# Kernel optimization log

Hardware: AMD Instinct MI355X
Metric: run time of the kernel (lower is better)

## Reference

```python
import jax, jax.numpy as jnp
import numpy as np

B, N, M = 4, 2048, 2048
QUERY_DIM = 512
CONTEXT_DIM = 512
HEADS = 8
DIM_HEAD = 64
INNER = HEADS * DIM_HEAD  # 512
SCALE = DIM_HEAD ** -0.5


def setup_inputs() -> dict:
    key = jax.random.key(0)
    ks = jax.random.split(key, 7)
    x = jax.random.normal(ks[0], (B, N, QUERY_DIM), dtype=jnp.float32)
    context = jax.random.normal(ks[1], (B, M, CONTEXT_DIM), dtype=jnp.float32)
    mask = jax.random.randint(ks[2], (B, M), 0, 2) > 0  # bool key mask
    # Kaiming-uniform-ish init scale, like nn.Linear defaults
    Wq = jax.random.uniform(ks[3], (QUERY_DIM, INNER), dtype=jnp.float32,
                            minval=-1, maxval=1) * (QUERY_DIM ** -0.5)
    Wkv = jax.random.uniform(ks[4], (CONTEXT_DIM, 2 * INNER), dtype=jnp.float32,
                             minval=-1, maxval=1) * (CONTEXT_DIM ** -0.5)
    Wo = jax.random.uniform(ks[5], (INNER, QUERY_DIM), dtype=jnp.float32,
                            minval=-1, maxval=1) * (INNER ** -0.5)
    bo = jax.random.uniform(ks[6], (QUERY_DIM,), dtype=jnp.float32,
                            minval=-1, maxval=1) * (INNER ** -0.5)
    return {"x": x, "context": context, "mask": mask,
            "Wq": Wq, "Wkv": Wkv, "Wo": Wo, "bo": bo}


def reference(x, context, mask, Wq, Wkv, Wo, bo):
    # projections (no bias for q/kv, bias for out — as in the torch module)
    q = x @ Wq                       # [b, n, inner]
    kv = context @ Wkv               # [b, m, 2*inner]
    k, v = jnp.split(kv, 2, axis=-1)
    # split heads: b n (h d) -> b h n d
    def split_heads(t):
        b, n, _ = t.shape
        return t.reshape(b, n, HEADS, DIM_HEAD).transpose(0, 2, 1, 3)
    q, k, v = split_heads(q), split_heads(k), split_heads(v)
    sim = jnp.einsum('bhid,bhjd->bhij', q, k) * SCALE  # [b, h, n, m]
    max_neg = -jnp.finfo(sim.dtype).max
    sim = jnp.where(mask[:, None, None, :], sim, max_neg)
    attn = jax.nn.softmax(sim, axis=-1)
    out = jnp.einsum('bhij,bhjd->bhid', attn, v)       # [b, h, n, d]
    out = out.transpose(0, 2, 1, 3).reshape(x.shape[0], x.shape[1], INNER)
    return out @ Wo + bo
```

## Files before the change

### kernel.cpp

```cpp
#include <hip/hip_runtime.h>
#include <hip/hip_bf16.h>
#include <cstddef>

typedef __attribute__((ext_vector_type(8))) short short8;
typedef __attribute__((ext_vector_type(4))) float f32x4;

__device__ inline unsigned short f2bf(float f) {
  unsigned int u = __float_as_uint(f);
  u += 0x7fffu + ((u >> 16) & 1u);
  return (unsigned short)(u >> 16);
}
__device__ inline unsigned int pkbf(float a, float b) {
  __hip_bfloat162 h = __float22bfloat162_rn(make_float2(a, b));
  union { __hip_bfloat162 h2; unsigned int u; } cv;
  cv.h2 = h;
  return cv.u;
}

__global__ __launch_bounds__(256) void prep_kernel(
    const float* __restrict__ Wq, const float* __restrict__ Wkv,
    const float* __restrict__ Wo, const int* __restrict__ mask,
    unsigned short* __restrict__ Wq_t, unsigned short* __restrict__ Wkv_t,
    unsigned short* __restrict__ Wo_t, unsigned int* __restrict__ pmask) {
  const int z = blockIdx.z;
  if (z == 3) {
    if (blockIdx.y != 0) return;
    int idx = blockIdx.x * 256 + threadIdx.x;
    int bb = idx >> 10, rem = idx & 1023;
    int g = rem >> 5, rem2 = rem & 31;
    int lqv = rem2 >> 3, e = rem2 & 7;
    int ct = e >> 1, half = e & 1;
    int key0 = g * 64 + half * 32 + lqv * 8 + 2 * ct;
    const int* mb = mask + bb * 2048;
    pmask[idx] = (mb[key0] ? 0xFFFFu : 0u) | (mb[key0 + 1] ? 0xFFFF0000u : 0u);
    return;
  }
  const float* src = (z == 0) ? Wq : (z == 1) ? Wkv : Wo;
  unsigned short* dst = (z == 0) ? Wq_t : (z == 1) ? Wkv_t : Wo_t;
  const int R = 512, C = (z == 1) ? 1024 : 512;
  if (blockIdx.x * 64 >= C) return;
  __shared__ float tile[64][65];
  int c0 = blockIdx.x * 64, r0 = blockIdx.y * 64;
  int tx = threadIdx.x & 63, ty = threadIdx.x >> 6;
  for (int i = ty; i < 64; i += 4)
    tile[i][tx] = src[(size_t)(r0 + i) * C + c0 + tx];
  __syncthreads();
  for (int i = ty; i < 64; i += 4)
    dst[(size_t)(c0 + i) * R + r0 + tx] = f2bf(tile[tx][i]);
}

__global__ __launch_bounds__(256) void proj_kernel(
    const float* __restrict__ x, const float* __restrict__ context,
    const unsigned short* __restrict__ Wq_t, const unsigned short* __restrict__ Wkv_t,
    unsigned short* __restrict__ qb, unsigned short* __restrict__ kb,
    unsigned short* __restrict__ vtb, float qscale) {
  __shared__ unsigned short As[128][72];
  __shared__ unsigned short Bs[128][72];
  const int bid = blockIdx.x;
  const bool isq = bid < 256;
  const float* Af = isq ? x : context;
  const unsigned short* Bt = isq ? Wq_t : Wkv_t;
  const int bn = (isq ? (bid & 3) : ((bid - 256) & 7)) * 128;
  const int bm = (isq ? (bid >> 2) : ((bid - 256) >> 3)) * 128;
  const int K = 512;
  const int tid = threadIdx.x;
  const int wave = tid >> 6, lane = tid & 63;
  const int wr = (wave >> 1) * 64, wc = (wave & 1) * 64;
  const int l15 = lane & 15, lq = lane >> 4;
  const int sr = tid >> 3, sc = (tid & 7) * 8;
  f32x4 acc[4][4] = {};

  for (int k0 = 0; k0 < K; k0 += 64) {
    __syncthreads();
#pragma unroll
    for (int p = 0; p < 4; ++p) {
      int r = sr + p * 32;
      const float4 f0 = *(const float4*)(Af + (size_t)(bm + r) * K + k0 + sc);
      const float4 f1 = *(const float4*)(Af + (size_t)(bm + r) * K + k0 + sc + 4);
      uint4 u;
      u.x = pkbf(f0.x, f0.y);
      u.y = pkbf(f0.z, f0.w);
      u.z = pkbf(f1.x, f1.y);
      u.w = pkbf(f1.z, f1.w);
      *(uint4*)(&As[r][sc]) = u;
      *(uint4*)(&Bs[r][sc]) = *(const uint4*)(Bt + (size_t)(bn + r) * K + k0 + sc);
    }
    __syncthreads();
#pragma unroll
    for (int kk = 0; kk < 2; ++kk) {
      short8 af[4], bfr[4];
#pragma unroll
      for (int mt = 0; mt < 4; ++mt)
        af[mt] = *(const short8*)(&As[wr + mt * 16 + l15][kk * 32 + lq * 8]);
#pragma unroll
      for (int nt = 0; nt < 4; ++nt)
        bfr[nt] = *(const short8*)(&Bs[wc + nt * 16 + l15][kk * 32 + lq * 8]);
#pragma unroll
      for (int mt = 0; mt < 4; ++mt)
#pragma unroll
        for (int nt = 0; nt < 4; ++nt)
          acc[mt][nt] = __builtin_amdgcn_mfma_f32_16x16x32_bf16(af[mt], bfr[nt], acc[mt][nt], 0, 0, 0);
    }
  }

#pragma unroll
  for (int mt = 0; mt < 4; ++mt)
#pragma unroll
    for (int nt = 0; nt < 4; ++nt) {
      int row0 = bm + wr + mt * 16 + lq * 4;
      int col = bn + wc + nt * 16 + l15;
      if (isq) {
#pragma unroll
        for (int j = 0; j < 4; ++j)
          qb[(size_t)(row0 + j) * 512 + col] = f2bf(acc[mt][nt][j] * qscale);
      } else if (col < 512) {
#pragma unroll
        for (int j = 0; j < 4; ++j)
          kb[(size_t)(row0 + j) * 512 + col] = f2bf(acc[mt][nt][j]);
      } else {
        int bb = row0 >> 11, m = row0 & 2047;
        int hd = col - 512;
        uint2 w;
        w.x = pkbf(acc[mt][nt][0], acc[mt][nt][1]);
        w.y = pkbf(acc[mt][nt][2], acc[mt][nt][3]);
        *(uint2*)(vtb + ((size_t)bb * 512 + hd) * 2048 + m) = w;
      }
    }
}

__global__ __launch_bounds__(256) void outproj_kernel(
    const unsigned short* __restrict__ Ab, const unsigned short* __restrict__ Bt,
    float* __restrict__ C0, const float* __restrict__ bias) {
  __shared__ unsigned short As[128][72];
  __shared__ unsigned short Bs[128][72];
  const int bm = blockIdx.y * 128, bn = blockIdx.x * 128;
  const int K = 512, N = 512;
  const int tid = threadIdx.x;
  const int wave = tid >> 6, lane = tid & 63;
  const int wr = (wave >> 1) * 64, wc = (wave & 1) * 64;
  const int l15 = lane & 15, lq = lane >> 4;
  const int sr = tid >> 3, sc = (tid & 7) * 8;
  f32x4 acc[4][4] = {};

  for (int k0 = 0; k0 < K; k0 += 64) {
    __syncthreads();
#pragma unroll
    for (int p = 0; p < 4; ++p) {
      int r = sr + p * 32;
      *(uint4*)(&As[r][sc]) = *(const uint4*)(Ab + (size_t)(bm + r) * K + k0 + sc);
      *(uint4*)(&Bs[r][sc]) = *(const uint4*)(Bt + (size_t)(bn + r) * K + k0 + sc);
    }
    __syncthreads();
#pragma unroll
    for (int kk = 0; kk < 2; ++kk) {
      short8 af[4], bfr[4];
#pragma unroll
      for (int mt = 0; mt < 4; ++mt)
        af[mt] = *(const short8*)(&As[wr + mt * 16 + l15][kk * 32 + lq * 8]);
#pragma unroll
      for (int nt = 0; nt < 4; ++nt)
        bfr[nt] = *(const short8*)(&Bs[wc + nt * 16 + l15][kk * 32 + lq * 8]);
#pragma unroll
      for (int mt = 0; mt < 4; ++mt)
#pragma unroll
        for (int nt = 0; nt < 4; ++nt)
          acc[mt][nt] = __builtin_amdgcn_mfma_f32_16x16x32_bf16(af[mt], bfr[nt], acc[mt][nt], 0, 0, 0);
    }
  }

#pragma unroll
  for (int mt = 0; mt < 4; ++mt)
#pragma unroll
    for (int nt = 0; nt < 4; ++nt) {
      int row0 = bm + wr + mt * 16 + lq * 4;
      int col = bn + wc + nt * 16 + l15;
#pragma unroll
      for (int j = 0; j < 4; ++j)
        C0[(size_t)(row0 + j) * N + col] = acc[mt][nt][j] + bias[col];
    }
}

__global__ __launch_bounds__(256, 2) void attn_kernel(
    const unsigned short* __restrict__ Q, const unsigned short* __restrict__ Kb,
    const unsigned short* __restrict__ Vt, const unsigned int* __restrict__ pmask,
    unsigned short* __restrict__ O) {
  __shared__ unsigned short Ks[2][2][64][72];
  __shared__ unsigned short Vs[2][2][64][72];
  const int b = blockIdx.x >> 3, h = blockIdx.x & 7;
  const int tid = threadIdx.x, lane = tid & 63;
  const int wave = tid >> 6;
  const int l15 = lane & 15, lq = lane >> 4;
  const int wrow = blockIdx.y * 128 + wave * 32;

  const unsigned short* Qr0 = Q + (size_t)(b * 2048 + wrow + l15) * 512 + h * 64;
  const unsigned short* Qr1 = Q + (size_t)(b * 2048 + wrow + 16 + l15) * 512 + h * 64;
  short8 q00 = *(const short8*)(Qr0 + lq * 8);
  short8 q01 = *(const short8*)(Qr0 + 32 + lq * 8);
  short8 q10 = *(const short8*)(Qr1 + lq * 8);
  short8 q11 = *(const short8*)(Qr1 + 32 + lq * 8);

  const short8 vones = {0x3F80, 0x3F80, 0x3F80, 0x3F80,
                        0x3F80, 0x3F80, 0x3F80, 0x3F80};

  f32x4 o0[4] = {}, o1[4] = {};
  f32x4 ol0 = {}, ol1 = {};

  const unsigned short* Kg = Kb + (size_t)b * 2048 * 512 + h * 64;
  const unsigned short* Vg = Vt + (size_t)(b * 8 + h) * 64 * 2048;
  const unsigned int* Pm = pmask + b * 1024;

  const int str = tid >> 3;
  const int stc = (tid & 7) * 8;
  const int kprow = ((str & 7) >> 1) * 16 + ((str >> 3) & 3) * 4 + (str & 1);

  uint4 krA0 = *(const uint4*)(Kg + (size_t)str * 512 + stc);
  uint4 krA1 = *(const uint4*)(Kg + (size_t)(str + 32) * 512 + stc);
  uint4 krB0 = *(const uint4*)(Kg + (size_t)(64 + str) * 512 + stc);
  uint4 krB1 = *(const uint4*)(Kg + (size_t)(64 + str + 32) * 512 + stc);
  uint4 vrA0 = *(const uint4*)(Vg + (size_t)str * 2048 + stc);
  uint4 vrA1 = *(const uint4*)(Vg + (size_t)(str + 32) * 2048 + stc);
  uint4 vrB0 = *(const uint4*)(Vg + (size_t)str * 2048 + 64 + stc);
  uint4 vrB1 = *(const uint4*)(Vg + (size_t)(str + 32) * 2048 + 64 + stc);
  uint4 pmA0 = *(const uint4*)(Pm + lq * 8);
  uint4 pmA1 = *(const uint4*)(Pm + lq * 8 + 4);
  uint4 pmB0 = *(const uint4*)(Pm + 32 + lq * 8);
  uint4 pmB1 = *(const uint4*)(Pm + 32 + lq * 8 + 4);

  for (int mb = 0; mb < 2048; mb += 128) {
    const int buf = (mb >> 7) & 1;
    *(uint4*)(&Ks[buf][0][kprow][stc])     = krA0;
    *(uint4*)(&Ks[buf][0][kprow + 2][stc]) = krA1;
    *(uint4*)(&Ks[buf][1][kprow][stc])     = krB0;
    *(uint4*)(&Ks[buf][1][kprow + 2][stc]) = krB1;
    *(uint4*)(&Vs[buf][0][str][stc])       = vrA0;
    *(uint4*)(&Vs[buf][0][str + 32][stc])  = vrA1;
    *(uint4*)(&Vs[buf][1][str][stc])       = vrB0;
    *(uint4*)(&Vs[buf][1][str + 32][stc])  = vrB1;
    uint4 pA0 = pmA0, pA1 = pmA1, pB0 = pmB0, pB1 = pmB1;
    __syncthreads();
    if (mb + 128 < 2048) {
      const int nx = mb + 128;
      krA0 = *(const uint4*)(Kg + (size_t)(nx + str) * 512 + stc);
      krA1 = *(const uint4*)(Kg + (size_t)(nx + str + 32) * 512 + stc);
      krB0 = *(const uint4*)(Kg + (size_t)(nx + 64 + str) * 512 + stc);
      krB1 = *(const uint4*)(Kg + (size_t)(nx + 64 + str + 32) * 512 + stc);
      vrA0 = *(const uint4*)(Vg + (size_t)str * 2048 + nx + stc);
      vrA1 = *(const uint4*)(Vg + (size_t)(str + 32) * 2048 + nx + stc);
      vrB0 = *(const uint4*)(Vg + (size_t)str * 2048 + nx + 64 + stc);
      vrB1 = *(const uint4*)(Vg + (size_t)(str + 32) * 2048 + nx + 64 + stc);
      pmA0 = *(const uint4*)(Pm + (nx >> 6) * 32 + lq * 8);
      pmA1 = *(const uint4*)(Pm + (nx >> 6) * 32 + lq * 8 + 4);
      pmB0 = *(const uint4*)(Pm + (nx >> 6) * 32 + 32 + lq * 8);
      pmB1 = *(const uint4*)(Pm + (nx >> 6) * 32 + 32 + lq * 8 + 4);
    }

#pragma unroll
    for (int g = 0; g < 2; ++g) {
      f32x4 s0[4] = {}, s1[4] = {};
#pragma unroll
      for (int ct = 0; ct < 4; ++ct) {
        short8 kf = *(const short8*)(&Ks[buf][g][ct * 16 + l15][lq * 8]);
        s0[ct] = __builtin_amdgcn_mfma_f32_16x16x32_bf16(kf, q00, s0[ct], 0, 0, 0);
        s1[ct] = __builtin_amdgcn_mfma_f32_16x16x32_bf16(kf, q10, s1[ct], 0, 0, 0);
      }
#pragma unroll
      for (int ct = 0; ct < 4; ++ct) {
        short8 kf = *(const short8*)(&Ks[buf][g][ct * 16 + l15][32 + lq * 8]);
        s0[ct] = __builtin_amdgcn_mfma_f32_16x16x32_bf16(kf, q01, s0[ct], 0, 0, 0);
        s1[ct] = __builtin_amdgcn_mfma_f32_16x16x32_bf16(kf, q11, s1[ct], 0, 0, 0);
      }

      unsigned int xp0[4][2], xp1[4][2];
#pragma unroll
      for (int ct = 0; ct < 4; ++ct) {
        float a0 = __builtin_amdgcn_exp2f(s0[ct][0]);
        float a1 = __builtin_amdgcn_exp2f(s0[ct][1]);
        float a2 = __builtin_amdgcn_exp2f(s0[ct][2]);
        float a3 = __builtin_amdgcn_exp2f(s0[ct][3]);
        xp0[ct][0] = pkbf(a0, a1);
        xp0[ct][1] = pkbf(a2, a3);
        float c0 = __builtin_amdgcn_exp2f(s1[ct][0]);
        float c1 = __builtin_amdgcn_exp2f(s1[ct][1]);
        float c2 = __builtin_amdgcn_exp2f(s1[ct][2]);
        float c3 = __builtin_amdgcn_exp2f(s1[ct][3]);
        xp1[ct][0] = pkbf(c0, c1);
        xp1[ct][1] = pkbf(c2, c3);
      }

      const uint4 m0 = g ? pB0 : pA0;
      const uint4 m1 = g ? pB1 : pA1;
      xp0[0][0] &= m0.x; xp0[0][1] &= m0.y; xp0[1][0] &= m0.z; xp0[1][1] &= m0.w;
      xp0[2][0] &= m1.x; xp0[2][1] &= m1.y; xp0[3][0] &= m1.z; xp0[3][1] &= m1.w;
      xp1[0][0] &= m0.x; xp1[0][1] &= m0.y; xp1[1][0] &= m0.z; xp1[1][1] &= m0.w;
      xp1[2][0] &= m1.x; xp1[2][1] &= m1.y; xp1[3][0] &= m1.z; xp1[3][1] &= m1.w;

#pragma unroll
      for (int kk = 0; kk < 2; ++kk) {
        union { unsigned int u[4]; short8 s8; } pc0, pc1;
        pc0.u[0] = xp0[0][kk]; pc0.u[1] = xp0[1][kk];
        pc0.u[2] = xp0[2][kk]; pc0.u[3] = xp0[3][kk];
        pc1.u[0] = xp1[0][kk]; pc1.u[1] = xp1[1][kk];
        pc1.u[2] = xp1[2][kk]; pc1.u[3] = xp1[3][kk];
#pragma unroll
        for (int dt = 0; dt < 4; ++dt) {
          short8 vf = *(const short8*)(&Vs[buf][g][dt * 16 + l15][kk * 32 + lq * 8]);
          o0[dt] = __builtin_amdgcn_mfma_f32_16x16x32_bf16(vf, pc0.s8, o0[dt], 0, 0, 0);
          o1[dt] = __builtin_amdgcn_mfma_f32_16x16x32_bf16(vf, pc1.s8, o1[dt], 0, 0, 0);
        }
        ol0 = __builtin_amdgcn_mfma_f32_16x16x32_bf16(vones, pc0.s8, ol0, 0, 0, 0);
        ol1 = __builtin_amdgcn_mfma_f32_16x16x32_bf16(vones, pc1.s8, ol1, 0, 0, 0);
      }
    }
  }

  float rl0 = 1.0f / ol0[0], rl1 = 1.0f / ol1[0];
  unsigned short* Or0 = O + (size_t)(b * 2048 + wrow + l15) * 512 + h * 64;
  unsigned short* Or1 = O + (size_t)(b * 2048 + wrow + 16 + l15) * 512 + h * 64;
#pragma unroll
  for (int dt = 0; dt < 4; ++dt) {
    *(unsigned int*)(Or0 + dt * 16 + lq * 4)     = pkbf(o0[dt][0] * rl0, o0[dt][1] * rl0);
    *(unsigned int*)(Or0 + dt * 16 + lq * 4 + 2) = pkbf(o0[dt][2] * rl0, o0[dt][3] * rl0);
    *(unsigned int*)(Or1 + dt * 16 + lq * 4)     = pkbf(o1[dt][0] * rl1, o1[dt][1] * rl1);
    *(unsigned int*)(Or1 + dt * 16 + lq * 4 + 2) = pkbf(o1[dt][2] * rl1, o1[dt][3] * rl1);
  }
}

extern "C" void kernel_launch(void* const* d_in, const int* in_sizes, int n_in,
                              void* d_out, int out_size, void* d_ws, size_t ws_size,
                              hipStream_t stream) {
  const float* x       = (const float*)d_in[0];
  const float* context = (const float*)d_in[1];
  const int*   mask    = (const int*)d_in[2];
  const float* Wq      = (const float*)d_in[3];
  const float* Wkv     = (const float*)d_in[4];
  const float* Wo      = (const float*)d_in[5];
  const float* bo      = (const float*)d_in[6];
  float* out = (float*)d_out;

  char* ws = (char*)d_ws;
  unsigned short* Wq_t  = (unsigned short*)(ws + 0);
  unsigned short* Wkv_t = (unsigned short*)(ws + 524288);
  unsigned short* Wo_t  = (unsigned short*)(ws + 1572864);
  unsigned short* qb    = (unsigned short*)(ws + 2097152);
  unsigned short* kb    = (unsigned short*)(ws + 10485760);
  unsigned short* vtb   = (unsigned short*)(ws + 18874368);
  unsigned short* ab    = (unsigned short*)(ws + 27262976);
  unsigned int* pmask   = (unsigned int*)(ws + 35651584);

  const float QSCALE = 0.125f * 1.44269504088896f;

  prep_kernel<<<dim3(16, 8, 4), 256, 0, stream>>>(Wq, Wkv, Wo, mask,
                                                  Wq_t, Wkv_t, Wo_t, pmask);
  proj_kernel<<<dim3(768), 256, 0, stream>>>(x, context, Wq_t, Wkv_t,
                                             qb, kb, vtb, QSCALE);
  attn_kernel<<<dim3(32, 16), 256, 0, stream>>>(qb, kb, vtb, pmask, ab);
  outproj_kernel<<<dim3(4, 64), 256, 0, stream>>>(ab, Wo_t, out, bo);
}
```

Measured before the change: 107.2 us.

## Single-buffer attention LDS and load mask per group to raise occupancy

The attention kernel drops LDS double buffering, halving shared memory to about 36KB, and adds a second barrier before the LDS writes. It also loads the mask words inside the inner loop instead of prefetching them into registers. Launch bounds move from 2 to 3 blocks per CU to allow more concurrent waves. The cost is an extra barrier per tile and exposed mask load latency, traded for higher occupancy and lower register pressure. The projection kernel gets a trivial index cleanup.

```diff
diff --git a/kernel.cpp b/kernel.cpp
--- a/kernel.cpp
+++ b/kernel.cpp
@@ -58,10 +58,11 @@
   __shared__ unsigned short Bs[128][72];
   const int bid = blockIdx.x;
   const bool isq = bid < 256;
+  const int lid = isq ? bid : bid - 256;
   const float* Af = isq ? x : context;
   const unsigned short* Bt = isq ? Wq_t : Wkv_t;
-  const int bn = (isq ? (bid & 3) : ((bid - 256) & 7)) * 128;
-  const int bm = (isq ? (bid >> 2) : ((bid - 256) >> 3)) * 128;
+  const int bn = (isq ? (lid & 3) : (lid & 7)) * 128;
+  const int bm = (isq ? (lid >> 2) : (lid >> 3)) * 128;
   const int K = 512;
   const int tid = threadIdx.x;
   const int wave = tid >> 6, lane = tid & 63;
@@ -180,12 +181,12 @@
     }
 }
 
-__global__ __launch_bounds__(256, 2) void attn_kernel(
+__global__ __launch_bounds__(256, 3) void attn_kernel(
     const unsigned short* __restrict__ Q, const unsigned short* __restrict__ Kb,
     const unsigned short* __restrict__ Vt, const unsigned int* __restrict__ pmask,
     unsigned short* __restrict__ O) {
-  __shared__ unsigned short Ks[2][2][64][72];
-  __shared__ unsigned short Vs[2][2][64][72];
+  __shared__ unsigned short Ks[2][64][72];
+  __shared__ unsigned short Vs[2][64][72];
   const int b = blockIdx.x >> 3, h = blockIdx.x & 7;
   const int tid = threadIdx.x, lane = tid & 63;
   const int wave = tid >> 6;
@@ -221,22 +222,17 @@
   uint4 vrA1 = *(const uint4*)(Vg + (size_t)(str + 32) * 2048 + stc);
   uint4 vrB0 = *(const uint4*)(Vg + (size_t)str * 2048 + 64 + stc);
   uint4 vrB1 = *(const uint4*)(Vg + (size_t)(str + 32) * 2048 + 64 + stc);
-  uint4 pmA0 = *(const uint4*)(Pm + lq * 8);
-  uint4 pmA1 = *(const uint4*)(Pm + lq * 8 + 4);
-  uint4 pmB0 = *(const uint4*)(Pm + 32 + lq * 8);
-  uint4 pmB1 = *(const uint4*)(Pm + 32 + lq * 8 + 4);
 
   for (int mb = 0; mb < 2048; mb += 128) {
-    const int buf = (mb >> 7) & 1;
-    *(uint4*)(&Ks[buf][0][kprow][stc])     = krA0;
-    *(uint4*)(&Ks[buf][0][kprow + 2][stc]) = krA1;
-    *(uint4*)(&Ks[buf][1][kprow][stc])     = krB0;
-    *(uint4*)(&Ks[buf][1][kprow + 2][stc]) = krB1;
-    *(uint4*)(&Vs[buf][0][str][stc])       = vrA0;
-    *(uint4*)(&Vs[buf][0][str + 32][stc])  = vrA1;
-    *(uint4*)(&Vs[buf][1][str][stc])       = vrB0;
-    *(uint4*)(&Vs[buf][1][str + 32][stc])  = vrB1;
-    uint4 pA0 = pmA0, pA1 = pmA1, pB0 = pmB0, pB1 = pmB1;
+    __syncthreads();
+    *(uint4*)(&Ks[0][kprow][stc])     = krA0;
+    *(uint4*)(&Ks[0][kprow + 2][stc]) = krA1;
+    *(uint4*)(&Ks[1][kprow][stc])     = krB0;
+    *(uint4*)(&Ks[1][kprow + 2][stc]) = krB1;
+    *(uint4*)(&Vs[0][str][stc])       = vrA0;
+    *(uint4*)(&Vs[0][str + 32][stc])  = vrA1;
+    *(uint4*)(&Vs[1][str][stc])       = vrB0;
+    *(uint4*)(&Vs[1][str + 32][stc])  = vrB1;
     __syncthreads();
     if (mb + 128 < 2048) {
       const int nx = mb + 128;
@@ -248,24 +244,23 @@
       vrA1 = *(const uint4*)(Vg + (size_t)(str + 32) * 2048 + nx + stc);
       vrB0 = *(const uint4*)(Vg + (size_t)str * 2048 + nx + 64 + stc);
       vrB1 = *(const uint4*)(Vg + (size_t)(str + 32) * 2048 + nx + 64 + stc);
-      pmA0 = *(const uint4*)(Pm + (nx >> 6) * 32 + lq * 8);
-      pmA1 = *(const uint4*)(Pm + (nx >> 6) * 32 + lq * 8 + 4);
-      pmB0 = *(const uint4*)(Pm + (nx >> 6) * 32 + 32 + lq * 8);
-      pmB1 = *(const uint4*)(Pm + (nx >> 6) * 32 + 32 + lq * 8 + 4);
     }
 
 #pragma unroll
     for (int g = 0; g < 2; ++g) {
+      const uint4 m0 = *(const uint4*)(Pm + ((mb >> 6) + g) * 32 + lq * 8);
+      const uint4 m1 = *(const uint4*)(Pm + ((mb >> 6) + g) * 32 + lq * 8 + 4);
+
       f32x4 s0[4] = {}, s1[4] = {};
 #pragma unroll
       for (int ct = 0; ct < 4; ++ct) {
-        short8 kf = *(const short8*)(&Ks[buf][g][ct * 16 + l15][lq * 8]);
+        short8 kf = *(const short8*)(&Ks[g][ct * 16 + l15][lq * 8]);
         s0[ct] = __builtin_amdgcn_mfma_f32_16x16x32_bf16(kf, q00, s0[ct], 0, 0, 0);
         s1[ct] = __builtin_amdgcn_mfma_f32_16x16x32_bf16(kf, q10, s1[ct], 0, 0, 0);
       }
 #pragma unroll
       for (int ct = 0; ct < 4; ++ct) {
-        short8 kf = *(const short8*)(&Ks[buf][g][ct * 16 + l15][32 + lq * 8]);
+        short8 kf = *(const short8*)(&Ks[g][ct * 16 + l15][32 + lq * 8]);
         s0[ct] = __builtin_amdgcn_mfma_f32_16x16x32_bf16(kf, q01, s0[ct], 0, 0, 0);
         s1[ct] = __builtin_amdgcn_mfma_f32_16x16x32_bf16(kf, q11, s1[ct], 0, 0, 0);
       }
@@ -287,8 +282,6 @@
         xp1[ct][1] = pkbf(c2, c3);
       }
 
-      const uint4 m0 = g ? pB0 : pA0;
-      const uint4 m1 = g ? pB1 : pA1;
       xp0[0][0] &= m0.x; xp0[0][1] &= m0.y; xp0[1][0] &= m0.z; xp0[1][1] &= m0.w;
       xp0[2][0] &= m1.x; xp0[2][1] &= m1.y; xp0[3][0] &= m1.z; xp0[3][1] &= m1.w;
       xp1[0][0] &= m0.x; xp1[0][1] &= m0.y; xp1[1][0] &= m0.z; xp1[1][1] &= m0.w;
@@ -303,7 +296,7 @@
         pc1.u[2] = xp1[2][kk]; pc1.u[3] = xp1[3][kk];
 #pragma unroll
         for (int dt = 0; dt < 4; ++dt) {
-          short8 vf = *(const short8*)(&Vs[buf][g][dt * 16 + l15][kk * 32 + lq * 8]);
+          short8 vf = *(const short8*)(&Vs[g][dt * 16 + l15][kk * 32 + lq * 8]);
           o0[dt] = __builtin_amdgcn_mfma_f32_16x16x32_bf16(vf, pc0.s8, o0[dt], 0, 0, 0);
           o1[dt] = __builtin_amdgcn_mfma_f32_16x16x32_bf16(vf, pc1.s8, o1[dt], 0, 0, 0);
         }
```

After: 107.4 us. No clear change (+0.2%).
